# Kernel optimization log

Hardware: AMD Instinct MI355X
Metric: run time of the kernel (lower is better)

The kernel has to match this reference:

```python
import jax, jax.numpy as jnp
import numpy as np

B, T, C, H = 4, 2048, 1024, 16
HD = C // H  # head_dim = 64


def _rope(x, cos, sin):
    # x: [B,H,T,HD]; cos/sin: [T,HD//2] -> broadcast [1,1,T,HD//2]
    x1 = x[..., 0::2]
    x2 = x[..., 1::2]
    cos = cos[None, None]
    sin = sin[None, None]
    o1 = x1 * cos - x2 * sin
    o2 = x1 * sin + x2 * cos
    # interleave back to [..., HD]
    return jnp.stack([o1, o2], axis=-1).reshape(x.shape)


def setup_inputs() -> dict:
    key = jax.random.key(0)
    ks = jax.random.split(key, 10)
    x = jax.random.normal(ks[0], (B, T, C), jnp.float32)
    # rotary frequencies (llama-style, theta=10000), stored as (cos,sin)
    inv_freq = 1.0 / (10000.0 ** (jnp.arange(0, HD, 2, dtype=jnp.float32) / HD))
    freqs = jnp.outer(jnp.arange(T, dtype=jnp.float32), inv_freq)  # [T, HD/2]
    freqs_cis = jnp.stack([jnp.cos(freqs), jnp.sin(freqs)], axis=-1)  # [T, HD/2, 2]
    attn_mask = jnp.tril(jnp.ones((T, T), jnp.int32))  # causal
    padding_mask = jnp.ones((B, T), jnp.int32)
    w = 0.02
    Wq = jax.random.normal(ks[1], (C, C), jnp.float32) * w
    Wk = jax.random.normal(ks[2], (C, C), jnp.float32) * w
    Wv = jax.random.normal(ks[3], (C, C), jnp.float32) * w
    Wp = jax.random.normal(ks[4], (C, C), jnp.float32) * w
    bq = jnp.zeros((C,), jnp.float32)
    bk = jnp.zeros((C,), jnp.float32)
    bv = jnp.zeros((C,), jnp.float32)
    bp = jnp.zeros((C,), jnp.float32)
    return {"x": x, "freqs_cis": freqs_cis, "attn_mask": attn_mask,
            "padding_mask": padding_mask, "Wq": Wq, "bq": bq, "Wk": Wk,
            "bk": bk, "Wv": Wv, "bv": bv, "Wp": Wp, "bp": bp}


def reference(x, freqs_cis, attn_mask, padding_mask, Wq, bq, Wk, bk, Wv, bv, Wp, bp):
    b, t, c = x.shape
    # qkv projections -> [B,H,T,HD]
    def heads(y):
        return y.reshape(b, t, H, HD).transpose(0, 2, 1, 3)
    q = heads(x @ Wq.T + bq)
    k = heads(x @ Wk.T + bk)
    v = heads(x @ Wv.T + bv)
    cos, sin = freqs_cis[..., 0], freqs_cis[..., 1]  # [T, HD/2]
    q = _rope(q, cos, sin)
    k = _rope(k, cos, sin)
    att = jnp.einsum('bhqd,bhkd->bhqk', q, k) * (1.0 / np.sqrt(HD).astype(np.float32))
    att = jnp.where(attn_mask[None, None] == 0, -1e30, att)
    att = jnp.where(padding_mask[:, None, None, :] == 0, -1e30, att)
    att = jax.nn.softmax(att, axis=-1)
    # dropout omitted (eval mode / deterministic reference)
    y = jnp.einsum('bhqk,bhkd->bhqd', att, v)
    y = y.transpose(0, 2, 1, 3).reshape(b, t, c)
    return y @ Wp.T + bp
```

## Files before the change

kernel.cpp:

```cpp
#include <hip/hip_runtime.h>
#include <hip/hip_bf16.h>

#define TB 2048
#define CC 1024
#define NH 16
#define HD 64
#define NB 4
#define BHX (NB*NH)
#define BTX (NB*TB)

typedef __attribute__((ext_vector_type(8))) short bf16x8;
typedef __attribute__((ext_vector_type(4))) float f32x4;
typedef __attribute__((ext_vector_type(4))) unsigned short us4;

__device__ __forceinline__ unsigned short bfb(float f) {
  __hip_bfloat16 h = __float2bfloat16(f);
  return __builtin_bit_cast(unsigned short, h);
}
__device__ __forceinline__ float fexp2(float x) {
  return __builtin_amdgcn_exp2f(x);
}
template <int CTRL>
__device__ __forceinline__ float dppf(float x) {
  int r = __builtin_amdgcn_update_dpp(0, __builtin_bit_cast(int, x), CTRL, 0xf, 0xf, false);
  return __builtin_bit_cast(float, r);
}

__device__ __forceinline__ void gld_lds16(const void* g, void* l) {
  __builtin_amdgcn_global_load_lds(
      (const __attribute__((address_space(1))) unsigned*)g,
      (__attribute__((address_space(3))) unsigned*)l, 16, 0, 0);
}

__global__ void cvt_f32_bf16(const float* __restrict__ src,
                             unsigned short* __restrict__ dst, int n4) {
  int i = blockIdx.x * blockDim.x + threadIdx.x;
  if (i >= n4) return;
  f32x4 v = ((const f32x4*)src)[i];
  us4 o;
#pragma unroll
  for (int j = 0; j < 4; j++) o[j] = bfb(v[j]);
  ((us4*)dst)[i] = o;
}

__global__ void cvt_w4(const float* __restrict__ s0, const float* __restrict__ s1,
                       const float* __restrict__ s2, const float* __restrict__ s3,
                       unsigned short* __restrict__ d0, unsigned short* __restrict__ d1,
                       unsigned short* __restrict__ d2, unsigned short* __restrict__ d3) {
  int y = blockIdx.y;
  const float* s = y == 0 ? s0 : y == 1 ? s1 : y == 2 ? s2 : s3;
  unsigned short* d = y == 0 ? d0 : y == 1 ? d1 : y == 2 ? d2 : d3;
  int i = blockIdx.x * 256 + threadIdx.x;
  f32x4 v = ((const f32x4*)s)[i];
  us4 o;
#pragma unroll
  for (int j = 0; j < 4; j++) o[j] = bfb(v[j]);
  ((us4*)d)[i] = o;
}

__global__ void prep_bias(const float* __restrict__ bq, const float* __restrict__ bk,
                          const float* __restrict__ bv, float* __restrict__ out) {
  int i = blockIdx.x * 256 + threadIdx.x;
  float v = i < 1024 ? bq[i] : i < 2048 ? bk[i - 1024] : bv[i - 2048];
  out[i] = v;
}

template <int MODE>
__global__ __launch_bounds__(256) void gemm_bt(
    const unsigned short* __restrict__ A, const unsigned short* __restrict__ Bw,
    const float* __restrict__ bias, const float* __restrict__ fcg,
    void* __restrict__ Cout, int M, int N, int K)
{
  __shared__ __align__(16) unsigned short As[128 * 32];
  __shared__ __align__(16) unsigned short Bs[128 * 32];
  int tid = threadIdx.x;
  int lane = tid & 63, wid = tid >> 6;
  int g = lane >> 4, l4 = lane & 15;
  int wr = wid >> 1, wc = wid & 1;
  int brow = blockIdx.y * 128, bcol = blockIdx.x * 128;

  const unsigned short* ap = A + (size_t)(brow + (tid >> 2)) * K + (tid & 3) * 8;
  const unsigned short* bp_ = Bw + (size_t)(bcol + (tid >> 2)) * K + (tid & 3) * 8;
  const size_t rstep = (size_t)64 * K;
  unsigned short* asl = As + tid * 8;
  unsigned short* bsl = Bs + tid * 8;

  f32x4 acc[4][4] = {};

  for (int k0 = 0; k0 < K; k0 += 32) {
    gld_lds16(ap, asl);
    gld_lds16(ap + rstep, asl + 2048);
    gld_lds16(bp_, bsl);
    gld_lds16(bp_ + rstep, bsl + 2048);
    ap += 32; bp_ += 32;
    __syncthreads();
    bf16x8 af[4], bfr[4];
#pragma unroll
    for (int i = 0; i < 4; i++)
      af[i] = *(const bf16x8*)&As[(wr * 64 + i * 16 + l4) * 32 + g * 8];
#pragma unroll
    for (int i = 0; i < 4; i++)
      bfr[i] = *(const bf16x8*)&Bs[(wc * 64 + i * 16 + l4) * 32 + g * 8];
#pragma unroll
    for (int i = 0; i < 4; i++)
#pragma unroll
      for (int j = 0; j < 4; j++)
        acc[i][j] = __builtin_amdgcn_mfma_f32_16x16x32_bf16(af[i], bfr[j], acc[i][j], 0, 0, 0);
    __syncthreads();
  }

#pragma unroll
  for (int i = 0; i < 4; i++) {
    int grow0 = brow + wr * 64 + i * 16 + 4 * g;
#pragma unroll
    for (int j = 0; j < 4; j++) {
      int gcol = bcol + wc * 64 + j * 16 + l4;
      float bv = bias[gcol];
      if (MODE == 0) {
        float* out = (float*)Cout;
#pragma unroll
        for (int r = 0; r < 4; r++)
          out[(size_t)(grow0 + r) * N + gcol] = acc[i][j][r] + bv;
      } else {
        unsigned short* out = (unsigned short*)Cout;
        int part = gcol >> 10;
        int c = gcol & 1023;
        int h = c >> 6, d = c & 63;
        int dbase = d & ~1;
        float sgn = (d & 1) ? 1.f : -1.f;
        bool isqk = (part < 2);
#pragma unroll
        for (int r = 0; r < 4; r++) {
          int grow = grow0 + r;
          int b = grow >> 11, t = grow & 2047;
          float v = acc[i][j][r] + bv;
          float w = __shfl_xor(v, 1, 64);
          float o = v;
          if (isqk) {
            float cth = fcg[(size_t)t * 64 + dbase];
            float sth = fcg[(size_t)t * 64 + dbase + 1];
            o = v * cth + sgn * w * sth;
          }
          size_t dst = (size_t)part * ((size_t)BHX * TB * HD)
                     + ((size_t)(b * NH + h) * TB + t) * HD + d;
          out[dst] = bfb(o);
        }
      }
    }
  }
}

__global__ void transpose_v(const unsigned short* __restrict__ v,
                            unsigned short* __restrict__ vT) {
  int bh = blockIdx.y, t0 = blockIdx.x * 64;
  __shared__ __align__(16) unsigned short tile[64][72];
  int tid = threadIdx.x;
#pragma unroll
  for (int s = 0; s < 2; s++) {
    int cid = tid + 256 * s;
    int r = cid >> 3, c8 = (cid & 7) * 8;
    bf16x8 val = *(const bf16x8*)(v + ((size_t)bh * TB + t0 + r) * HD + c8);
    *(bf16x8*)&tile[r][c8] = val;
  }
  __syncthreads();
#pragma unroll
  for (int s = 0; s < 2; s++) {
    int cid = tid + 256 * s;
    int rr = cid >> 3, cc = (cid & 7) * 8;
    bf16x8 o;
#pragma unroll
    for (int i = 0; i < 8; i++) o[i] = (short)tile[cc + i][rr];
    *(bf16x8*)(vT + ((size_t)bh * HD + rr) * TB + t0 + cc) = o;
  }
}

__global__ __launch_bounds__(256, 4) void flash_fwd(
    const unsigned short* __restrict__ q, const unsigned short* __restrict__ k,
    const unsigned short* __restrict__ vT, unsigned short* __restrict__ yb)
{
  __shared__ __align__(16) unsigned short Ks[2][4096];
  __shared__ __align__(16) unsigned short Vs[2][4096];
  __shared__ __align__(16) unsigned short Ps[4][16][64];

  const int tid = threadIdx.x, wid = tid >> 6, lane = tid & 63;
  const int g = lane >> 4, l4 = lane & 15;

  const int b = blockIdx.x;
  const int xcd = b & 7;
  const int idx = b >> 3;
  const int bh = (xcd << 3) | (idx & 7);
  const int p = idx >> 3;

  const int off0 = tid << 4;
  const int row0 = off0 >> 7, sc0 = ((off0 >> 4) & 7) ^ (row0 & 7);
  const int off1 = off0 + 4096;
  const int row1 = off1 >> 7, sc1 = ((off1 >> 4) & 7) ^ (row1 & 7);
  const int koff0 = (row0 << 6) + (sc0 << 3);
  const int koff1 = (row1 << 6) + (sc1 << 3);
  const int voff0 = (row0 << 11) + (sc0 << 3);
  const int voff1 = (row1 << 11) + (sc1 << 3);

  const float SCL2 = 0.18033688011112042f;

  const unsigned short* kb = k  + ((size_t)bh << 17);
  const unsigned short* vb = vT + ((size_t)bh << 17);

#pragma unroll 1
  for (int sel = 0; sel < 2; sel++) {
    const int q64 = sel ? (31 - p) : p;
    const int rbase = q64 * 64 + wid * 16;

    bf16x8 qf0, qf1;
    {
      const unsigned short* qp = q + (((size_t)bh * TB + rbase + l4) << 6);
      qf0 = *(const bf16x8*)(qp + g * 8);
      qf1 = *(const bf16x8*)(qp + 32 + g * 8);
    }

    float m_run[4], l_run[4];
    f32x4 acc_o[4] = {};
#pragma unroll
    for (int j = 0; j < 4; j++) { m_run[j] = -1e30f; l_run[j] = 0.f; }

    gld_lds16(kb + koff0, &Ks[0][off0 >> 1]);
    gld_lds16(kb + koff1, &Ks[0][off1 >> 1]);
    gld_lds16(vb + voff0, &Vs[0][off0 >> 1]);
    gld_lds16(vb + voff1, &Vs[0][off1 >> 1]);
    __syncthreads();

    for (int kt = 0; kt <= q64; kt++) {
      const int cur = kt & 1;
      if (kt < q64) {
        const int kadd = (kt + 1) << 12;
        const int vadd = (kt + 1) << 6;
        gld_lds16(kb + koff0 + kadd, &Ks[cur ^ 1][off0 >> 1]);
        gld_lds16(kb + koff1 + kadd, &Ks[cur ^ 1][off1 >> 1]);
        gld_lds16(vb + voff0 + vadd, &Vs[cur ^ 1][off0 >> 1]);
        gld_lds16(vb + voff1 + vadd, &Vs[cur ^ 1][off1 >> 1]);
      }
      const unsigned short* Kc = Ks[cur];
      const unsigned short* Vc = Vs[cur];

      float sv[4][4];
      __builtin_amdgcn_s_setprio(1);
#pragma unroll
      for (int cb = 0; cb < 4; cb++) {
        const int r = cb * 16 + l4;
        const int sw = (r & 7) * 8;
        bf16x8 kb0 = *(const bf16x8*)&Kc[r * 64 + ((g * 8) ^ sw)];
        bf16x8 kb1 = *(const bf16x8*)&Kc[r * 64 + (((g + 4) * 8) ^ sw)];
        f32x4 z = {0.f, 0.f, 0.f, 0.f};
        z = __builtin_amdgcn_mfma_f32_16x16x32_bf16(qf0, kb0, z, 0, 0, 0);
        z = __builtin_amdgcn_mfma_f32_16x16x32_bf16(qf1, kb1, z, 0, 0, 0);
#pragma unroll
        for (int j = 0; j < 4; j++)
          sv[cb][j] = z[j] * SCL2;
      }
      __builtin_amdgcn_s_setprio(0);
      if (kt == q64) {
        const int rq = wid * 16 + 4 * g;
#pragma unroll
        for (int cb = 0; cb < 4; cb++)
#pragma unroll
          for (int j = 0; j < 4; j++)
            if (cb * 16 + l4 > rq + j) sv[cb][j] = -1e30f;
      }

      float mt[4];
#pragma unroll
      for (int j = 0; j < 4; j++) {
        float m = fmaxf(fmaxf(sv[0][j], sv[1][j]), fmaxf(sv[2][j], sv[3][j]));
        m = fmaxf(m, dppf<0x121>(m));
        m = fmaxf(m, dppf<0x122>(m));
        m = fmaxf(m, dppf<0x124>(m));
        m = fmaxf(m, dppf<0x128>(m));
        mt[j] = m;
      }
      bool need = !((mt[0] <= m_run[0] + 8.f) & (mt[1] <= m_run[1] + 8.f) &
                    (mt[2] <= m_run[2] + 8.f) & (mt[3] <= m_run[3] + 8.f));
      if (__any(need)) {
#pragma unroll
        for (int j = 0; j < 4; j++) {
          float mn = fmaxf(m_run[j], mt[j]);
          float alpha = fexp2(m_run[j] - mn);
          m_run[j] = mn;
          l_run[j] *= alpha;
#pragma unroll
          for (int db = 0; db < 4; db++) acc_o[db][j] *= alpha;
        }
      }
#pragma unroll
      for (int j = 0; j < 4; j++) {
        float s0 = fexp2(sv[0][j] - m_run[j]); sv[0][j] = s0;
        float s1 = fexp2(sv[1][j] - m_run[j]); sv[1][j] = s1;
        float s2 = fexp2(sv[2][j] - m_run[j]); sv[2][j] = s2;
        float s3 = fexp2(sv[3][j] - m_run[j]); sv[3][j] = s3;
        float p2 = (s0 + s1) + (s2 + s3);
        p2 += dppf<0x121>(p2);
        p2 += dppf<0x122>(p2);
        p2 += dppf<0x124>(p2);
        p2 += dppf<0x128>(p2);
        l_run[j] += p2;
      }

#pragma unroll
      for (int cb = 0; cb < 4; cb++)
#pragma unroll
        for (int j = 0; j < 4; j++) {
          const int xch = (cb * 2 + (l4 >> 3)) ^ ((g & 1) * 4 + j);
          Ps[wid][4 * g + j][xch * 8 + (l4 & 7)] = bfb(sv[cb][j]);
        }
      asm volatile("s_waitcnt lgkmcnt(0)" ::: "memory");
      __builtin_amdgcn_sched_barrier(0);
      bf16x8 pa0 = *(const bf16x8*)&Ps[wid][l4][(g ^ (l4 & 7)) * 8];
      bf16x8 pa1 = *(const bf16x8*)&Ps[wid][l4][((4 + g) ^ (l4 & 7)) * 8];
      __builtin_amdgcn_s_setprio(1);
#pragma unroll
      for (int db = 0; db < 4; db++) {
        const int r = db * 16 + l4;
        const int sw = (r & 7) * 8;
        bf16x8 vb0 = *(const bf16x8*)&Vc[r * 64 + ((g * 8) ^ sw)];
        bf16x8 vb1 = *(const bf16x8*)&Vc[r * 64 + (((g + 4) * 8) ^ sw)];
        acc_o[db] = __builtin_amdgcn_mfma_f32_16x16x32_bf16(pa0, vb0, acc_o[db], 0, 0, 0);
        acc_o[db] = __builtin_amdgcn_mfma_f32_16x16x32_bf16(pa1, vb1, acc_o[db], 0, 0, 0);
      }
      __builtin_amdgcn_s_setprio(0);
      __syncthreads();
    }

    unsigned short* yp = yb + ((size_t)(bh >> 4) * TB) * CC + (size_t)(bh & 15) * HD;
    const int qr0 = rbase + 4 * g;
    float inv[4];
#pragma unroll
    for (int j = 0; j < 4; j++) inv[j] = 1.0f / l_run[j];
#pragma unroll
    for (int db = 0; db < 4; db++) {
      const int d = db * 16 + l4;
#pragma unroll
      for (int j = 0; j < 4; j++)
        yp[(size_t)(qr0 + j) * CC + d] = bfb(acc_o[db][j] * inv[j]);
    }
  }
}

extern "C" void kernel_launch(void* const* d_in, const int* in_sizes, int n_in,
                              void* d_out, int out_size, void* d_ws, size_t ws_size,
                              hipStream_t stream) {
  (void)in_sizes; (void)n_in; (void)out_size; (void)ws_size;
  const float* x  = (const float*)d_in[0];
  const float* fc = (const float*)d_in[1];
  const float* Wq = (const float*)d_in[4];
  const float* bq = (const float*)d_in[5];
  const float* Wk = (const float*)d_in[6];
  const float* bk = (const float*)d_in[7];
  const float* Wv = (const float*)d_in[8];
  const float* bv = (const float*)d_in[9];
  const float* Wp = (const float*)d_in[10];
  const float* bp = (const float*)d_in[11];

  char* ws = (char*)d_ws;
  unsigned short* xb   = (unsigned short*)(ws + 0);
  unsigned short* wqkv = (unsigned short*)(ws + 16777216);
  unsigned short* wp   = (unsigned short*)(ws + 23068672);
  float*          bqkv = (float*)(ws + 25165824);
  unsigned short* qkv  = (unsigned short*)(ws + 25182208);
  unsigned short* vT   = qkv + 3 * (size_t)8388608;
  unsigned short* yb   = xb;

  cvt_f32_bf16<<<(2097152 + 255) / 256, 256, 0, stream>>>(x, xb, 2097152);
  cvt_w4<<<dim3(1024, 4), 256, 0, stream>>>(Wq, Wk, Wv, Wp,
      wqkv, wqkv + 1048576, wqkv + 2097152, wp);
  prep_bias<<<dim3(12), 256, 0, stream>>>(bq, bk, bv, bqkv);

  gemm_bt<1><<<dim3(24, 64), 256, 0, stream>>>(xb, wqkv, bqkv, fc, qkv, BTX, 3072, 1024);
  transpose_v<<<dim3(32, 64), 256, 0, stream>>>(qkv + 2 * (size_t)8388608, vT);
  flash_fwd<<<dim3(1024), 256, 0, stream>>>(qkv, qkv + (size_t)8388608, vT, yb);
  gemm_bt<0><<<dim3(8, 64), 256, 0, stream>>>(yb, wp, bp, nullptr, (float*)d_out, BTX, 1024, 1024);
}
```

Baseline: 234.1 us.

## Double-buffer GEMM LDS tiles, swizzle block order for XCDs, raise MFMA priority

The GEMM kernel now uses two LDS buffers so the next K-slice's global-to-LDS load is issued before computing on the current slice, removing one barrier per iteration. The 2D grid becomes a 1D grid whose block index is remapped so that consecutive blocks landing on the same XCD cover nearby tiles, which should improve L2 reuse. s_setprio is raised around the MFMA burst. LDS usage doubles per block, which may lower occupancy.

```diff
diff --git a/kernel.cpp b/kernel.cpp
--- a/kernel.cpp
+++ b/kernel.cpp
@@ -69,43 +69,57 @@
 __global__ __launch_bounds__(256) void gemm_bt(
     const unsigned short* __restrict__ A, const unsigned short* __restrict__ Bw,
     const float* __restrict__ bias, const float* __restrict__ fcg,
-    void* __restrict__ Cout, int M, int N, int K)
+    void* __restrict__ Cout, int M, int N, int K, int nbx)
 {
-  __shared__ __align__(16) unsigned short As[128 * 32];
-  __shared__ __align__(16) unsigned short Bs[128 * 32];
+  __shared__ __align__(16) unsigned short As[2][4096];
+  __shared__ __align__(16) unsigned short Bs[2][4096];
   int tid = threadIdx.x;
   int lane = tid & 63, wid = tid >> 6;
   int g = lane >> 4, l4 = lane & 15;
   int wr = wid >> 1, wc = wid & 1;
-  int brow = blockIdx.y * 128, bcol = blockIdx.x * 128;
+  const int cpx = gridDim.x >> 3;
+  const int swz = (blockIdx.x & 7) * cpx + (blockIdx.x >> 3);
+  const int bx = swz % nbx, by = swz / nbx;
+  const int brow = by * 128, bcol = bx * 128;
 
   const unsigned short* ap = A + (size_t)(brow + (tid >> 2)) * K + (tid & 3) * 8;
   const unsigned short* bp_ = Bw + (size_t)(bcol + (tid >> 2)) * K + (tid & 3) * 8;
   const size_t rstep = (size_t)64 * K;
-  unsigned short* asl = As + tid * 8;
-  unsigned short* bsl = Bs + tid * 8;
+  const int lo = tid * 8;
 
   f32x4 acc[4][4] = {};
 
-  for (int k0 = 0; k0 < K; k0 += 32) {
-    gld_lds16(ap, asl);
-    gld_lds16(ap + rstep, asl + 2048);
-    gld_lds16(bp_, bsl);
-    gld_lds16(bp_ + rstep, bsl + 2048);
-    ap += 32; bp_ += 32;
-    __syncthreads();
+  gld_lds16(ap,          &As[0][lo]);
+  gld_lds16(ap + rstep,  &As[0][lo + 2048]);
+  gld_lds16(bp_,         &Bs[0][lo]);
+  gld_lds16(bp_ + rstep, &Bs[0][lo + 2048]);
+  ap += 32; bp_ += 32;
+  __syncthreads();
+
+  const int nk = K >> 5;
+  for (int kk = 0; kk < nk; kk++) {
+    const int cur = kk & 1;
+    if (kk + 1 < nk) {
+      gld_lds16(ap,          &As[cur ^ 1][lo]);
+      gld_lds16(ap + rstep,  &As[cur ^ 1][lo + 2048]);
+      gld_lds16(bp_,         &Bs[cur ^ 1][lo]);
+      gld_lds16(bp_ + rstep, &Bs[cur ^ 1][lo + 2048]);
+      ap += 32; bp_ += 32;
+    }
     bf16x8 af[4], bfr[4];
 #pragma unroll
     for (int i = 0; i < 4; i++)
-      af[i] = *(const bf16x8*)&As[(wr * 64 + i * 16 + l4) * 32 + g * 8];
+      af[i] = *(const bf16x8*)&As[cur][(wr * 64 + i * 16 + l4) * 32 + g * 8];
 #pragma unroll
     for (int i = 0; i < 4; i++)
-      bfr[i] = *(const bf16x8*)&Bs[(wc * 64 + i * 16 + l4) * 32 + g * 8];
+      bfr[i] = *(const bf16x8*)&Bs[cur][(wc * 64 + i * 16 + l4) * 32 + g * 8];
+    __builtin_amdgcn_s_setprio(1);
 #pragma unroll
     for (int i = 0; i < 4; i++)
 #pragma unroll
       for (int j = 0; j < 4; j++)
         acc[i][j] = __builtin_amdgcn_mfma_f32_16x16x32_bf16(af[i], bfr[j], acc[i][j], 0, 0, 0);
+    __builtin_amdgcn_s_setprio(0);
     __syncthreads();
   }
 
@@ -372,8 +386,8 @@
       wqkv, wqkv + 1048576, wqkv + 2097152, wp);
   prep_bias<<<dim3(12), 256, 0, stream>>>(bq, bk, bv, bqkv);
 
-  gemm_bt<1><<<dim3(24, 64), 256, 0, stream>>>(xb, wqkv, bqkv, fc, qkv, BTX, 3072, 1024);
+  gemm_bt<1><<<dim3(1536), 256, 0, stream>>>(xb, wqkv, bqkv, fc, qkv, BTX, 3072, 1024, 24);
   transpose_v<<<dim3(32, 64), 256, 0, stream>>>(qkv + 2 * (size_t)8388608, vT);
   flash_fwd<<<dim3(1024), 256, 0, stream>>>(qkv, qkv + (size_t)8388608, vT, yb);
-  gemm_bt<0><<<dim3(8, 64), 256, 0, stream>>>(yb, wp, bp, nullptr, (float*)d_out, BTX, 1024, 1024);
-}
+  gemm_bt<0><<<dim3(512), 256, 0, stream>>>(yb, wp, bp, nullptr, (float*)d_out, BTX, 1024, 1024, 8);
+}
```

Result: faster. 221.7 us (-5.3%).

## Replace GEMM with 256x128 triple-buffered, swizzled-LDS, 8-wave pipelined kernel

Applied to the files above, without the earlier changes.

Rewrites the projection GEMMs to use 512-thread blocks with 256x128 tiles and a K-step of 64. Tiles are staged through a three-deep LDS ring with direct global-to-LDS loads issued two steps ahead, so memory traffic overlaps the MFMA work. The LDS layout uses an XOR swizzle to avoid bank conflicts, blocks are remapped across XCDs for L2 locality, and s_setprio raises priority around MFMA bursts. The cost is much more LDS per block (about 144KB), which may limit occupancy, and K is hardcoded to 1024.

```diff
diff --git a/kernel.cpp b/kernel.cpp
--- a/kernel.cpp
+++ b/kernel.cpp
@@ -66,83 +66,155 @@
 }
 
 template <int MODE>
-__global__ __launch_bounds__(256) void gemm_bt(
+__global__ __launch_bounds__(512) void gemm8(
     const unsigned short* __restrict__ A, const unsigned short* __restrict__ Bw,
     const float* __restrict__ bias, const float* __restrict__ fcg,
-    void* __restrict__ Cout, int M, int N, int K)
+    void* __restrict__ Cout, int N, int nbx)
 {
-  __shared__ __align__(16) unsigned short As[128 * 32];
-  __shared__ __align__(16) unsigned short Bs[128 * 32];
-  int tid = threadIdx.x;
-  int lane = tid & 63, wid = tid >> 6;
-  int g = lane >> 4, l4 = lane & 15;
-  int wr = wid >> 1, wc = wid & 1;
-  int brow = blockIdx.y * 128, bcol = blockIdx.x * 128;
-
-  const unsigned short* ap = A + (size_t)(brow + (tid >> 2)) * K + (tid & 3) * 8;
-  const unsigned short* bp_ = Bw + (size_t)(bcol + (tid >> 2)) * K + (tid & 3) * 8;
-  const size_t rstep = (size_t)64 * K;
-  unsigned short* asl = As + tid * 8;
-  unsigned short* bsl = Bs + tid * 8;
+  const int K = 1024;
+  __shared__ __align__(16) unsigned short As[3][16384];
+  __shared__ __align__(16) unsigned short Bs[3][8192];
+  const int tid = threadIdx.x;
+  const int lane = tid & 63, wid = tid >> 6;
+  const int g = lane >> 4, l4 = lane & 15;
+  const int wr = wid >> 1, wc = wid & 1;
+  const int cpx = gridDim.x >> 3;
+  const int swz = (blockIdx.x & 7) * cpx + (blockIdx.x >> 3);
+  const int bx = swz % nbx, by = swz / nbx;
+  const int brow = by * 256, bcol = bx * 128;
+
+  const unsigned short* asrc[4];
+  int adst[4];
+#pragma unroll
+  for (int s = 0; s < 4; s++) {
+    int cid = tid + 512 * s;
+    int row = cid >> 3, sc = (cid & 7) ^ (row & 7);
+    asrc[s] = A + (size_t)(brow + row) * K + sc * 8;
+    adst[s] = cid * 8;
+  }
+  const unsigned short* bsrc[2];
+  int bdst[2];
+#pragma unroll
+  for (int s = 0; s < 2; s++) {
+    int cid = tid + 512 * s;
+    int row = cid >> 3, sc = (cid & 7) ^ (row & 7);
+    bsrc[s] = Bw + (size_t)(bcol + row) * K + sc * 8;
+    bdst[s] = cid * 8;
+  }
+
+  int ar[4], br[4];
+#pragma unroll
+  for (int i = 0; i < 4; i++) {
+    ar[i] = (wr * 64 + i * 16 + l4) * 64;
+    br[i] = (wc * 64 + i * 16 + l4) * 64;
+  }
+  const int sl0 = ((g) ^ (l4 & 7)) * 8;
+  const int sl1 = ((4 + g) ^ (l4 & 7)) * 8;
 
   f32x4 acc[4][4] = {};
 
-  for (int k0 = 0; k0 < K; k0 += 32) {
-    gld_lds16(ap, asl);
-    gld_lds16(ap + rstep, asl + 2048);
-    gld_lds16(bp_, bsl);
-    gld_lds16(bp_ + rstep, bsl + 2048);
-    ap += 32; bp_ += 32;
-    __syncthreads();
-    bf16x8 af[4], bfr[4];
-#pragma unroll
-    for (int i = 0; i < 4; i++)
-      af[i] = *(const bf16x8*)&As[(wr * 64 + i * 16 + l4) * 32 + g * 8];
-#pragma unroll
-    for (int i = 0; i < 4; i++)
-      bfr[i] = *(const bf16x8*)&Bs[(wc * 64 + i * 16 + l4) * 32 + g * 8];
-#pragma unroll
-    for (int i = 0; i < 4; i++)
-#pragma unroll
-      for (int j = 0; j < 4; j++)
-        acc[i][j] = __builtin_amdgcn_mfma_f32_16x16x32_bf16(af[i], bfr[j], acc[i][j], 0, 0, 0);
-    __syncthreads();
-  }
-
-#pragma unroll
-  for (int i = 0; i < 4; i++) {
-    int grow0 = brow + wr * 64 + i * 16 + 4 * g;
-#pragma unroll
-    for (int j = 0; j < 4; j++) {
-      int gcol = bcol + wc * 64 + j * 16 + l4;
+#pragma unroll
+  for (int s = 0; s < 4; s++) gld_lds16(asrc[s], &As[0][adst[s]]);
+#pragma unroll
+  for (int s = 0; s < 2; s++) gld_lds16(bsrc[s], &Bs[0][bdst[s]]);
+#pragma unroll
+  for (int s = 0; s < 4; s++) gld_lds16(asrc[s] + 64, &As[1][adst[s]]);
+#pragma unroll
+  for (int s = 0; s < 2; s++) gld_lds16(bsrc[s] + 64, &Bs[1][bdst[s]]);
+  asm volatile("s_waitcnt vmcnt(6)" ::: "memory");
+  __builtin_amdgcn_s_barrier();
+  __builtin_amdgcn_sched_barrier(0);
+
+  const int nt = K >> 6;
+  int c = 0;
+  for (int t = 0; t < nt; t++) {
+    const unsigned short* Ac = As[c];
+    const unsigned short* Bc = Bs[c];
+    {
+      bf16x8 af[4], bf[4];
+#pragma unroll
+      for (int mf = 0; mf < 4; mf++) af[mf] = *(const bf16x8*)&Ac[ar[mf] + sl0];
+#pragma unroll
+      for (int nf = 0; nf < 4; nf++) bf[nf] = *(const bf16x8*)&Bc[br[nf] + sl0];
+      __builtin_amdgcn_s_setprio(1);
+#pragma unroll
+      for (int mf = 0; mf < 4; mf++)
+#pragma unroll
+        for (int nf = 0; nf < 4; nf++)
+          acc[mf][nf] = __builtin_amdgcn_mfma_f32_16x16x32_bf16(af[mf], bf[nf], acc[mf][nf], 0, 0, 0);
+      __builtin_amdgcn_s_setprio(0);
+      asm volatile("" ::: "memory");
+      __builtin_amdgcn_s_barrier();
+      __builtin_amdgcn_sched_barrier(0);
+    }
+    {
+      if (t + 2 < nt) {
+        int c2 = c + 2; if (c2 >= 3) c2 -= 3;
+        const int ko = (t + 2) << 6;
+#pragma unroll
+        for (int s = 0; s < 4; s++) gld_lds16(asrc[s] + ko, &As[c2][adst[s]]);
+#pragma unroll
+        for (int s = 0; s < 2; s++) gld_lds16(bsrc[s] + ko, &Bs[c2][bdst[s]]);
+      }
+      bf16x8 af[4], bf[4];
+#pragma unroll
+      for (int mf = 0; mf < 4; mf++) af[mf] = *(const bf16x8*)&Ac[ar[mf] + sl1];
+#pragma unroll
+      for (int nf = 0; nf < 4; nf++) bf[nf] = *(const bf16x8*)&Bc[br[nf] + sl1];
+      __builtin_amdgcn_s_setprio(1);
+#pragma unroll
+      for (int mf = 0; mf < 4; mf++)
+#pragma unroll
+        for (int nf = 0; nf < 4; nf++)
+          acc[mf][nf] = __builtin_amdgcn_mfma_f32_16x16x32_bf16(af[mf], bf[nf], acc[mf][nf], 0, 0, 0);
+      __builtin_amdgcn_s_setprio(0);
+      if (t + 2 < nt)
+        asm volatile("s_waitcnt vmcnt(6)" ::: "memory");
+      else if (t + 1 < nt)
+        asm volatile("s_waitcnt vmcnt(0)" ::: "memory");
+      if (t + 1 < nt) {
+        asm volatile("" ::: "memory");
+        __builtin_amdgcn_s_barrier();
+        __builtin_amdgcn_sched_barrier(0);
+      }
+    }
+    c = (c == 2) ? 0 : c + 1;
+  }
+
+#pragma unroll
+  for (int mf = 0; mf < 4; mf++) {
+    int grow0 = brow + wr * 64 + mf * 16 + 4 * g;
+#pragma unroll
+    for (int nf = 0; nf < 4; nf++) {
+      int gcol = bcol + wc * 64 + nf * 16 + l4;
       float bv = bias[gcol];
       if (MODE == 0) {
         float* out = (float*)Cout;
 #pragma unroll
         for (int r = 0; r < 4; r++)
-          out[(size_t)(grow0 + r) * N + gcol] = acc[i][j][r] + bv;
+          out[(size_t)(grow0 + r) * N + gcol] = acc[mf][nf][r] + bv;
       } else {
         unsigned short* out = (unsigned short*)Cout;
         int part = gcol >> 10;
-        int c = gcol & 1023;
-        int h = c >> 6, d = c & 63;
+        int cc2 = gcol & 1023;
+        int h = cc2 >> 6, d = cc2 & 63;
         int dbase = d & ~1;
         float sgn = (d & 1) ? 1.f : -1.f;
         bool isqk = (part < 2);
 #pragma unroll
         for (int r = 0; r < 4; r++) {
           int grow = grow0 + r;
-          int b = grow >> 11, t = grow & 2047;
-          float v = acc[i][j][r] + bv;
+          int b = grow >> 11, tt = grow & 2047;
+          float v = acc[mf][nf][r] + bv;
           float w = __shfl_xor(v, 1, 64);
           float o = v;
           if (isqk) {
-            float cth = fcg[(size_t)t * 64 + dbase];
-            float sth = fcg[(size_t)t * 64 + dbase + 1];
+            float cth = fcg[(size_t)tt * 64 + dbase];
+            float sth = fcg[(size_t)tt * 64 + dbase + 1];
             o = v * cth + sgn * w * sth;
           }
           size_t dst = (size_t)part * ((size_t)BHX * TB * HD)
-                     + ((size_t)(b * NH + h) * TB + t) * HD + d;
+                     + ((size_t)(b * NH + h) * TB + tt) * HD + d;
           out[dst] = bfb(o);
         }
       }
@@ -372,8 +444,8 @@
       wqkv, wqkv + 1048576, wqkv + 2097152, wp);
   prep_bias<<<dim3(12), 256, 0, stream>>>(bq, bk, bv, bqkv);
 
-  gemm_bt<1><<<dim3(24, 64), 256, 0, stream>>>(xb, wqkv, bqkv, fc, qkv, BTX, 3072, 1024);
+  gemm8<1><<<dim3(768), 512, 0, stream>>>(xb, wqkv, bqkv, fc, qkv, 3072, 24);
   transpose_v<<<dim3(32, 64), 256, 0, stream>>>(qkv + 2 * (size_t)8388608, vT);
   flash_fwd<<<dim3(1024), 256, 0, stream>>>(qkv, qkv + (size_t)8388608, vT, yb);
-  gemm_bt<0><<<dim3(8, 64), 256, 0, stream>>>(yb, wp, bp, nullptr, (float*)d_out, BTX, 1024, 1024);
-}
+  gemm8<0><<<dim3(256), 512, 0, stream>>>(yb, wp, bp, nullptr, (float*)d_out, 1024, 8);
+}
```

After: 241.6 us. 3.2% more time.
